# Optimization experiments

Hardware: AMD Instinct MI355X
Metric: run time of the kernel (lower is better)

The kernel has to match this reference:

```python
import jax, jax.numpy as jnp
import numpy as np

N = 50000
E = 800000
F_IN = 128
HID = 128
NCLS = 64


def setup_inputs() -> dict:
    key = jax.random.key(0)
    ks = jax.random.split(key, 10)
    x = jax.random.normal(ks[0], (N, F_IN), dtype=jnp.float32)
    edge_index = jax.random.randint(ks[1], (2, E), 0, N, dtype=jnp.int64)
    def w(k, fi, fo):
        return jax.random.normal(k, (fi, fo), dtype=jnp.float32) / np.sqrt(fi)
    return {
        "x": x,
        "edge_index": edge_index,
        "W1": w(ks[2], F_IN, HID), "b1": jnp.zeros((HID,), jnp.float32),
        "W2": w(ks[3], HID, HID), "b2": jnp.zeros((HID,), jnp.float32),
        "W3": w(ks[4], HID, HID), "b3": jnp.zeros((HID,), jnp.float32),
        "W4": w(ks[5], HID, NCLS), "b4": jnp.zeros((NCLS,), jnp.float32),
    }


def _build_graph(edge_index, n):
    # PyG GCNConv default: add self loops, symmetric normalization D^-1/2 (A+I) D^-1/2
    loops = jnp.arange(n, dtype=edge_index.dtype)
    row = jnp.concatenate([edge_index[0], loops])  # source
    col = jnp.concatenate([edge_index[1], loops])  # destination
    deg = jax.ops.segment_sum(jnp.ones_like(col, dtype=jnp.float32), col, num_segments=n)
    dinv = jnp.where(deg > 0, jax.lax.rsqrt(deg), 0.0)
    norm = dinv[row] * dinv[col]  # [E+N]
    return row, col, norm


def _gcn_layer(x, row, col, norm, W, b, n):
    h = x @ W                                    # [N, out]
    msg = h[row] * norm[:, None]                 # gather + scale, [E+N, out]
    out = jax.ops.segment_sum(msg, col, num_segments=n)  # scatter-add
    return out + b


def reference(x, edge_index, W1, b1, W2, b2, W3, b3, W4, b4):
    n = x.shape[0]
    row, col, norm = _build_graph(edge_index, n)
    h = jax.nn.relu(_gcn_layer(x, row, col, norm, W1, b1, n))
    h = jax.nn.relu(_gcn_layer(h, row, col, norm, W2, b2, n))
    h = jax.nn.relu(_gcn_layer(h, row, col, norm, W3, b3, n))
    return _gcn_layer(h, row, col, norm, W4, b4, n)
```

## Files before the change

### kernel.cpp

```cpp
#include <hip/hip_runtime.h>
#include <hip/hip_fp16.h>
#include <type_traits>

#define N_NODES 50000
#define N_EDGES 800000
#define WIN_BITS 9
#define WIN 512
#define NBUK ((N_NODES + WIN - 1) / WIN)
#define BCAP 16384

typedef _Float16 half8 __attribute__((ext_vector_type(8)));
typedef float floatx4 __attribute__((ext_vector_type(4)));

__global__ __launch_bounds__(256) void p0_bucket(const int* __restrict__ ei,
                                                 int* __restrict__ gcur,
                                                 unsigned* __restrict__ arena, int E) {
    __shared__ int lcnt[NBUK];
    __shared__ int lbase[NBUK];
    int tid = threadIdx.x;
    int chunk = (E + gridDim.x - 1) / gridDim.x;
    int e0 = blockIdx.x * chunk;
    int e1 = e0 + chunk; if (e1 > E) e1 = E;
    for (int b = tid; b < NBUK; b += 256) lcnt[b] = 0;
    __syncthreads();
    for (int e = e0 + tid; e < e1; e += 256) {
        int dst = ei[E + e];
        atomicAdd(&lcnt[dst >> WIN_BITS], 1);
    }
    __syncthreads();
    for (int b = tid; b < NBUK; b += 256) {
        lbase[b] = atomicAdd(&gcur[b], lcnt[b]);
        lcnt[b] = 0;
    }
    __syncthreads();
    for (int e = e0 + tid; e < e1; e += 256) {
        int dst = ei[E + e];
        int src = ei[e];
        int b = dst >> WIN_BITS;
        int pos = lbase[b] + atomicAdd(&lcnt[b], 1);
        if (pos < BCAP)
            arena[(size_t)b * BCAP + pos] = ((unsigned)src << WIN_BITS) | (unsigned)(dst & (WIN - 1));
    }
}

__global__ __launch_bounds__(256) void p1_count(const unsigned* __restrict__ arena,
                                                const int* __restrict__ gcur,
                                                int* __restrict__ deg,
                                                float* __restrict__ dinv, int n) {
    __shared__ int cnt[WIN];
    int b = blockIdx.x, tid = threadIdx.x;
    for (int j = tid; j < WIN; j += 256) cnt[j] = 0;
    __syncthreads();
    int m = gcur[b]; if (m > BCAP) m = BCAP;
    const unsigned* a = arena + (size_t)b * BCAP;
    for (int i = tid; i < m; i += 256) atomicAdd(&cnt[a[i] & (WIN - 1)], 1);
    __syncthreads();
    int base = b << WIN_BITS;
    for (int j = tid; j < WIN; j += 256) {
        int d = base + j;
        if (d < n) {
            int c = cnt[j];
            deg[d] = c;
            dinv[d] = rsqrtf((float)(c + 1));
        }
    }
}

__global__ __launch_bounds__(256) void scan_blocksum(const int* __restrict__ deg,
                                                     int* __restrict__ blocksum, int n) {
    int tid = threadIdx.x;
    int i0 = blockIdx.x * 1024 + tid * 4;
    int4 d = make_int4(0, 0, 0, 0);
    if (i0 + 3 < n) d = *(const int4*)&deg[i0];
    else {
        if (i0 < n)     d.x = deg[i0];
        if (i0 + 1 < n) d.y = deg[i0 + 1];
        if (i0 + 2 < n) d.z = deg[i0 + 2];
        if (i0 + 3 < n) d.w = deg[i0 + 3];
    }
    int s = d.x + d.y + d.z + d.w;
    #pragma unroll
    for (int off = 1; off < 64; off <<= 1) s += __shfl_xor(s, off);
    __shared__ int ws[4];
    if ((tid & 63) == 0) ws[tid >> 6] = s;
    __syncthreads();
    if (tid == 0) blocksum[blockIdx.x] = ws[0] + ws[1] + ws[2] + ws[3];
}

__global__ void scan_blockoff(const int* __restrict__ blocksum, int* __restrict__ blockoff,
                              int nb, int* __restrict__ offsets, int n, int total) {
    int lane = threadIdx.x;
    int v = (lane < nb) ? blocksum[lane] : 0;
    int orig = v;
    #pragma unroll
    for (int off = 1; off < 64; off <<= 1) {
        int t = __shfl_up(v, off);
        if (lane >= off) v += t;
    }
    if (lane < nb) blockoff[lane] = v - orig;
    if (lane == 0) offsets[n] = total;
}

__global__ __launch_bounds__(256) void scan_fill(const int* __restrict__ deg,
                                                 const int* __restrict__ blockoff,
                                                 int* __restrict__ offsets, int n) {
    int tid = threadIdx.x;
    int i0 = blockIdx.x * 1024 + tid * 4;
    int4 d = make_int4(0, 0, 0, 0);
    if (i0 + 3 < n) d = *(const int4*)&deg[i0];
    else {
        if (i0 < n)     d.x = deg[i0];
        if (i0 + 1 < n) d.y = deg[i0 + 1];
        if (i0 + 2 < n) d.z = deg[i0 + 2];
        if (i0 + 3 < n) d.w = deg[i0 + 3];
    }
    int ts = d.x + d.y + d.z + d.w;
    __shared__ int sbuf[256];
    sbuf[tid] = ts;
    __syncthreads();
    #pragma unroll
    for (int off = 1; off < 256; off <<= 1) {
        int t = (tid >= off) ? sbuf[tid - off] : 0;
        __syncthreads();
        sbuf[tid] += t;
        __syncthreads();
    }
    int base = blockoff[blockIdx.x] + (sbuf[tid] - ts);
    int o0 = base, o1 = o0 + d.x, o2 = o1 + d.y, o3 = o2 + d.z;
    if (i0 + 3 < n) {
        *(int4*)&offsets[i0] = make_int4(o0, o1, o2, o3);
    } else {
        if (i0 < n)     offsets[i0]     = o0;
        if (i0 + 1 < n) offsets[i0 + 1] = o1;
        if (i0 + 2 < n) offsets[i0 + 2] = o2;
    }
}

__global__ __launch_bounds__(256) void p2_fill(const unsigned* __restrict__ arena,
                                               const int* __restrict__ gcur,
                                               const int* __restrict__ offsets,
                                               int* __restrict__ csr_src, int n) {
    __shared__ int cur[WIN];
    int b = blockIdx.x, tid = threadIdx.x;
    int base = b << WIN_BITS;
    for (int j = tid; j < WIN; j += 256) {
        int d = base + j;
        cur[j] = (d < n) ? offsets[d] : 0;
    }
    __syncthreads();
    int m = gcur[b]; if (m > BCAP) m = BCAP;
    const unsigned* a = arena + (size_t)b * BCAP;
    for (int i = tid; i < m; i += 256) {
        unsigned e = a[i];
        int pos = atomicAdd(&cur[e & (WIN - 1)], 1);
        csr_src[pos] = (int)(e >> WIN_BITS);
    }
}

template<int FO, typename InT>
__global__ __launch_bounds__(256) void gemm_mfma_kernel(
        const InT* __restrict__ x, const float* __restrict__ W,
        const float* __restrict__ dinv, __half* __restrict__ h, int n) {
    constexpr int NT = FO / 16;
    __shared__ _Float16 wlds[4 * 4 * FO * 8];

    int tid = threadIdx.x;
    constexpr int G = 4 * 4 * FO;
    for (int it = 0; it < G / 256; ++it) {
        int g = tid + it * 256;
        int col = g % FO;
        int sq = g / FO;
        int k0 = sq * 8;
        half8 hv;
        #pragma unroll
        for (int j = 0; j < 8; ++j)
            hv[j] = (_Float16)W[(size_t)(k0 + j) * FO + col];
        *(half8*)&wlds[(size_t)g * 8] = hv;
    }
    __syncthreads();

    int ln = tid & 15;
    int q  = (tid >> 4) & 3;
    int w  = tid >> 6;
    int node = blockIdx.x * 64 + w * 16 + ln;
    int nodec = node < n ? node : n - 1;
    const InT* xrow = x + (size_t)nodec * 128;

    floatx4 acc[NT];
    #pragma unroll
    for (int t = 0; t < NT; ++t) acc[t] = (floatx4){0.f, 0.f, 0.f, 0.f};

    #pragma unroll
    for (int s = 0; s < 4; ++s) {
        half8 xf;
        if constexpr (std::is_same_v<InT, float>) {
            const float* xp = xrow + s * 32 + q * 8;
            float4 a0 = *(const float4*)xp;
            float4 a1 = *(const float4*)(xp + 4);
            xf[0] = (_Float16)a0.x; xf[1] = (_Float16)a0.y;
            xf[2] = (_Float16)a0.z; xf[3] = (_Float16)a0.w;
            xf[4] = (_Float16)a1.x; xf[5] = (_Float16)a1.y;
            xf[6] = (_Float16)a1.z; xf[7] = (_Float16)a1.w;
        } else {
            xf = *(const half8*)(xrow + s * 32 + q * 8);
        }
        int sq = s * 4 + q;
        #pragma unroll
        for (int t = 0; t < NT; ++t) {
            half8 wf = *(const half8*)&wlds[(size_t)(sq * FO + t * 16 + ln) * 8];
            acc[t] = __builtin_amdgcn_mfma_f32_16x16x32_f16(wf, xf, acc[t], 0, 0, 0);
        }
    }

    if (node < n) {
        float dv = dinv[node];
        __half* hrow = h + (size_t)node * FO;
        #pragma unroll
        for (int t = 0; t < NT; ++t) {
            __half2 p[2];
            p[0] = __float22half2_rn(make_float2(acc[t][0] * dv, acc[t][1] * dv));
            p[1] = __float22half2_rn(make_float2(acc[t][2] * dv, acc[t][3] * dv));
            *(uint2*)&hrow[t * 16 + q * 4] = *(const uint2*)p;
        }
    }
}

template<typename OutT, bool RELU>
__global__ __launch_bounds__(256) void agg128_kernel(
        const __half2* __restrict__ h2, const int* __restrict__ offsets,
        const int* __restrict__ csr_src, const float* __restrict__ dinv,
        const float* __restrict__ bias, OutT* __restrict__ out, int n) {
    int lane = threadIdx.x & 63;
    int c = (blockIdx.x << 2) + (threadIdx.x >> 6);
    if (c >= n) return;
    c = __builtin_amdgcn_readfirstlane(c);
    float2 acc = __half22float2(h2[(size_t)c * 64 + lane]);
    int s = offsets[c], e = offsets[c + 1];
    int i = s;
    for (; i + 3 < e; i += 4) {
        int s0 = csr_src[i], s1 = csr_src[i + 1], s2 = csr_src[i + 2], s3 = csr_src[i + 3];
        float2 f0 = __half22float2(h2[(size_t)s0 * 64 + lane]);
        float2 f1 = __half22float2(h2[(size_t)s1 * 64 + lane]);
        float2 f2 = __half22float2(h2[(size_t)s2 * 64 + lane]);
        float2 f3 = __half22float2(h2[(size_t)s3 * 64 + lane]);
        acc.x += f0.x + f1.x; acc.y += f0.y + f1.y;
        acc.x += f2.x + f3.x; acc.y += f2.y + f3.y;
    }
    for (; i < e; ++i) {
        float2 f = __half22float2(h2[(size_t)csr_src[i] * 64 + lane]);
        acc.x += f.x; acc.y += f.y;
    }
    float dc = dinv[c];
    float2 bb = ((const float2*)bias)[lane];
    float vx = fmaf(acc.x, dc, bb.x);
    float vy = fmaf(acc.y, dc, bb.y);
    if (RELU) { vx = fmaxf(vx, 0.0f); vy = fmaxf(vy, 0.0f); }
    if constexpr (std::is_same_v<OutT, __half>) {
        ((__half2*)out)[(size_t)c * 64 + lane] = __float22half2_rn(make_float2(vx, vy));
    } else {
        float2 o; o.x = vx; o.y = vy;
        ((float2*)out)[(size_t)c * 64 + lane] = o;
    }
}

__global__ __launch_bounds__(256) void agg64_kernel(
        const __half2* __restrict__ h2, const int* __restrict__ offsets,
        const int* __restrict__ csr_src, const float* __restrict__ dinv,
        const float* __restrict__ bias, float* __restrict__ out, int n) {
    int lane = threadIdx.x & 63;
    int hf = lane >> 5, sl = lane & 31;
    int c = (blockIdx.x << 2) + (threadIdx.x >> 6);
    if (c >= n) return;
    c = __builtin_amdgcn_readfirstlane(c);
    float2 acc = make_float2(0.0f, 0.0f);
    if (hf == 0) acc = __half22float2(h2[(size_t)c * 32 + sl]);
    int s = offsets[c], e = offsets[c + 1];
    int i = s;
    for (; i + 3 < e; i += 4) {
        int sa = csr_src[i + hf];
        int sb = csr_src[i + 2 + hf];
        float2 fa = __half22float2(h2[(size_t)sa * 32 + sl]);
        float2 fb = __half22float2(h2[(size_t)sb * 32 + sl]);
        acc.x += fa.x + fb.x; acc.y += fa.y + fb.y;
    }
    for (; i + 1 < e; i += 2) {
        int sa = csr_src[i + hf];
        float2 fa = __half22float2(h2[(size_t)sa * 32 + sl]);
        acc.x += fa.x; acc.y += fa.y;
    }
    if (i < e && hf == 0) {
        float2 fa = __half22float2(h2[(size_t)csr_src[i] * 32 + sl]);
        acc.x += fa.x; acc.y += fa.y;
    }
    acc.x += __shfl_xor(acc.x, 32);
    acc.y += __shfl_xor(acc.y, 32);
    if (hf == 0) {
        float dc = dinv[c];
        float2 bb = ((const float2*)bias)[sl];
        float2 o;
        o.x = fmaf(acc.x, dc, bb.x);
        o.y = fmaf(acc.y, dc, bb.y);
        ((float2*)out)[(size_t)c * 32 + sl] = o;
    }
}


extern "C" void kernel_launch(void* const* d_in, const int* in_sizes, int n_in,
                              void* d_out, int out_size, void* d_ws, size_t ws_size,
                              hipStream_t stream) {
    const float* x  = (const float*)d_in[0];
    const int*   ei = (const int*)  d_in[1];
    const float* W1 = (const float*)d_in[2];
    const float* b1 = (const float*)d_in[3];
    const float* W2 = (const float*)d_in[4];
    const float* b2 = (const float*)d_in[5];
    const float* W3 = (const float*)d_in[6];
    const float* b3 = (const float*)d_in[7];
    const float* W4 = (const float*)d_in[8];
    const float* b4 = (const float*)d_in[9];

    const int N = N_NODES, E = N_EDGES;
    const int NSB = (N + 1023) / 1024;

    char* p = (char*)d_ws;
    auto carve = [&](size_t bytes) {
        char* q = p;
        p += (bytes + 255) & ~(size_t)255;
        return (void*)q;
    };
    int*      deg      = (int*)     carve((size_t)N * 4);
    int*      offsets  = (int*)     carve((size_t)(N + 1) * 4);
    int*      csr_src  = (int*)     carve((size_t)E * 4);
    float*    dinv     = (float*)   carve((size_t)N * 4);
    int*      blocksum = (int*)     carve((size_t)NSB * 4);
    int*      blockoff = (int*)     carve((size_t)NSB * 4);
    int*      gcur     = (int*)     carve((size_t)NBUK * 4);
    unsigned* arena    = (unsigned*)carve((size_t)NBUK * BCAP * 4);
    __half*   A        = (__half*)  carve((size_t)N * 128 * 2);
    __half*   B        = (__half*)  carve((size_t)N * 128 * 2);

    hipMemsetAsync(gcur, 0, (size_t)NBUK * 4, stream);
    p0_bucket<<<512, 256, 0, stream>>>(ei, gcur, arena, E);
    p1_count<<<NBUK, 256, 0, stream>>>(arena, gcur, deg, dinv, N);
    scan_blocksum<<<NSB, 256, 0, stream>>>(deg, blocksum, N);
    scan_blockoff<<<1, 64, 0, stream>>>(blocksum, blockoff, NSB, offsets, N, E);
    scan_fill<<<NSB, 256, 0, stream>>>(deg, blockoff, offsets, N);
    p2_fill<<<NBUK, 256, 0, stream>>>(arena, gcur, offsets, csr_src, N);

    const int gemm_grid = (N + 63) / 64;
    const int agg_grid  = (N + 3) / 4;

    gemm_mfma_kernel<128, float><<<gemm_grid, 256, 0, stream>>>(x, W1, dinv, A, N);
    agg128_kernel<__half, true><<<agg_grid, 256, 0, stream>>>((const __half2*)A, offsets, csr_src, dinv, b1, B, N);
    gemm_mfma_kernel<128, __half><<<gemm_grid, 256, 0, stream>>>(B, W2, dinv, A, N);
    agg128_kernel<__half, true><<<agg_grid, 256, 0, stream>>>((const __half2*)A, offsets, csr_src, dinv, b2, B, N);
    gemm_mfma_kernel<128, __half><<<gemm_grid, 256, 0, stream>>>(B, W3, dinv, A, N);
    agg128_kernel<__half, true><<<agg_grid, 256, 0, stream>>>((const __half2*)A, offsets, csr_src, dinv, b3, B, N);
    gemm_mfma_kernel<64, __half><<<gemm_grid, 256, 0, stream>>>(B, W4, dinv, A, N);
    agg64_kernel<<<agg_grid, 256, 0, stream>>>((const __half2*)A, offsets, csr_src, dinv, b4, (float*)d_out, N);
}
```

Before: 312.8 us.

## Fuse aggregation with next-layer MFMA GEMM and merge degree scan into bucket count

Each hidden-layer aggregation (gather-sum, scale, bias, ReLU) now writes its 64-node tile to LDS, and the same 512-thread block runs the next layer's MFMA GEMM on it. This removes the fp16 round trip of the intermediate activations through global memory and three kernel launches. CSR offset construction now scans per-bucket counts in one small kernel and does the per-node prefix inside the count kernel, replacing the three-kernel deg/blocksum/fill scan. The cost is fewer, larger blocks for the gather phase (8 nodes per wave serially), which reduces the memory-level parallelism available to the latency-bound gathers, plus higher LDS use per block.

```diff
diff --git a/kernel.cpp b/kernel.cpp
--- a/kernel.cpp
+++ b/kernel.cpp
@@ -43,96 +43,58 @@
     }
 }
 
-__global__ __launch_bounds__(256) void p1_count(const unsigned* __restrict__ arena,
-                                                const int* __restrict__ gcur,
-                                                int* __restrict__ deg,
-                                                float* __restrict__ dinv, int n) {
+__global__ void scan_buckets(const int* __restrict__ gcur, int* __restrict__ bukoff,
+                             int* __restrict__ offsets, int n, int total) {
+    __shared__ int s[128];
+    int t = threadIdx.x;
+    int v = (t < NBUK) ? gcur[t] : 0;
+    s[t] = v;
+    __syncthreads();
+    for (int off = 1; off < 128; off <<= 1) {
+        int u = (t >= off) ? s[t - off] : 0;
+        __syncthreads();
+        s[t] += u;
+        __syncthreads();
+    }
+    if (t < NBUK) bukoff[t] = s[t] - v;
+    if (t == 0) offsets[n] = total;
+}
+
+__global__ __launch_bounds__(256) void p1_count_scan(const unsigned* __restrict__ arena,
+                                                     const int* __restrict__ gcur,
+                                                     const int* __restrict__ bukoff,
+                                                     int* __restrict__ offsets,
+                                                     float* __restrict__ dinv, int n) {
     __shared__ int cnt[WIN];
+    __shared__ int sbuf[256];
     int b = blockIdx.x, tid = threadIdx.x;
-    for (int j = tid; j < WIN; j += 256) cnt[j] = 0;
+    cnt[tid] = 0; cnt[tid + 256] = 0;
     __syncthreads();
     int m = gcur[b]; if (m > BCAP) m = BCAP;
     const unsigned* a = arena + (size_t)b * BCAP;
     for (int i = tid; i < m; i += 256) atomicAdd(&cnt[a[i] & (WIN - 1)], 1);
     __syncthreads();
+    int j0 = tid * 2;
+    int a0 = cnt[j0], a1 = cnt[j0 + 1];
+    int ts = a0 + a1;
+    sbuf[tid] = ts;
+    __syncthreads();
+    for (int off = 1; off < 256; off <<= 1) {
+        int u = (tid >= off) ? sbuf[tid - off] : 0;
+        __syncthreads();
+        sbuf[tid] += u;
+        __syncthreads();
+    }
+    int pre = sbuf[tid] - ts;
     int base = b << WIN_BITS;
-    for (int j = tid; j < WIN; j += 256) {
-        int d = base + j;
-        if (d < n) {
-            int c = cnt[j];
-            deg[d] = c;
-            dinv[d] = rsqrtf((float)(c + 1));
-        }
-    }
-}
-
-__global__ __launch_bounds__(256) void scan_blocksum(const int* __restrict__ deg,
-                                                     int* __restrict__ blocksum, int n) {
-    int tid = threadIdx.x;
-    int i0 = blockIdx.x * 1024 + tid * 4;
-    int4 d = make_int4(0, 0, 0, 0);
-    if (i0 + 3 < n) d = *(const int4*)&deg[i0];
-    else {
-        if (i0 < n)     d.x = deg[i0];
-        if (i0 + 1 < n) d.y = deg[i0 + 1];
-        if (i0 + 2 < n) d.z = deg[i0 + 2];
-        if (i0 + 3 < n) d.w = deg[i0 + 3];
-    }
-    int s = d.x + d.y + d.z + d.w;
-    #pragma unroll
-    for (int off = 1; off < 64; off <<= 1) s += __shfl_xor(s, off);
-    __shared__ int ws[4];
-    if ((tid & 63) == 0) ws[tid >> 6] = s;
-    __syncthreads();
-    if (tid == 0) blocksum[blockIdx.x] = ws[0] + ws[1] + ws[2] + ws[3];
-}
-
-__global__ void scan_blockoff(const int* __restrict__ blocksum, int* __restrict__ blockoff,
-                              int nb, int* __restrict__ offsets, int n, int total) {
-    int lane = threadIdx.x;
-    int v = (lane < nb) ? blocksum[lane] : 0;
-    int orig = v;
-    #pragma unroll
-    for (int off = 1; off < 64; off <<= 1) {
-        int t = __shfl_up(v, off);
-        if (lane >= off) v += t;
-    }
-    if (lane < nb) blockoff[lane] = v - orig;
-    if (lane == 0) offsets[n] = total;
-}
-
-__global__ __launch_bounds__(256) void scan_fill(const int* __restrict__ deg,
-                                                 const int* __restrict__ blockoff,
-                                                 int* __restrict__ offsets, int n) {
-    int tid = threadIdx.x;
-    int i0 = blockIdx.x * 1024 + tid * 4;
-    int4 d = make_int4(0, 0, 0, 0);
-    if (i0 + 3 < n) d = *(const int4*)&deg[i0];
-    else {
-        if (i0 < n)     d.x = deg[i0];
-        if (i0 + 1 < n) d.y = deg[i0 + 1];
-        if (i0 + 2 < n) d.z = deg[i0 + 2];
-        if (i0 + 3 < n) d.w = deg[i0 + 3];
-    }
-    int ts = d.x + d.y + d.z + d.w;
-    __shared__ int sbuf[256];
-    sbuf[tid] = ts;
-    __syncthreads();
-    #pragma unroll
-    for (int off = 1; off < 256; off <<= 1) {
-        int t = (tid >= off) ? sbuf[tid - off] : 0;
-        __syncthreads();
-        sbuf[tid] += t;
-        __syncthreads();
-    }
-    int base = blockoff[blockIdx.x] + (sbuf[tid] - ts);
-    int o0 = base, o1 = o0 + d.x, o2 = o1 + d.y, o3 = o2 + d.z;
-    if (i0 + 3 < n) {
-        *(int4*)&offsets[i0] = make_int4(o0, o1, o2, o3);
-    } else {
-        if (i0 < n)     offsets[i0]     = o0;
-        if (i0 + 1 < n) offsets[i0 + 1] = o1;
-        if (i0 + 2 < n) offsets[i0 + 2] = o2;
+    int o0 = bukoff[b] + pre, o1 = o0 + a0;
+    int d0 = base + j0;
+    if (d0 + 1 < n) {
+        *(int2*)&offsets[d0] = make_int2(o0, o1);
+        *(float2*)&dinv[d0] = make_float2(rsqrtf((float)(a0 + 1)), rsqrtf((float)(a1 + 1)));
+    } else if (d0 < n) {
+        offsets[d0] = o0;
+        dinv[d0] = rsqrtf((float)(a0 + 1));
     }
 }
 
@@ -162,10 +124,10 @@
         const InT* __restrict__ x, const float* __restrict__ W,
         const float* __restrict__ dinv, __half* __restrict__ h, int n) {
     constexpr int NT = FO / 16;
-    __shared__ _Float16 wlds[4 * 4 * FO * 8];
+    __shared__ _Float16 wlds[16 * FO * 8];
 
     int tid = threadIdx.x;
-    constexpr int G = 4 * 4 * FO;
+    constexpr int G = 16 * FO;
     for (int it = 0; it < G / 256; ++it) {
         int g = tid + it * 256;
         int col = g % FO;
@@ -225,41 +187,95 @@
     }
 }
 
-template<typename OutT, bool RELU>
-__global__ __launch_bounds__(256) void agg128_kernel(
-        const __half2* __restrict__ h2, const int* __restrict__ offsets,
+template<int FO>
+__global__ __launch_bounds__(512) void fused_agg_gemm(
+        const __half2* __restrict__ hin, const int* __restrict__ offsets,
         const int* __restrict__ csr_src, const float* __restrict__ dinv,
-        const float* __restrict__ bias, OutT* __restrict__ out, int n) {
-    int lane = threadIdx.x & 63;
-    int c = (blockIdx.x << 2) + (threadIdx.x >> 6);
-    if (c >= n) return;
-    c = __builtin_amdgcn_readfirstlane(c);
-    float2 acc = __half22float2(h2[(size_t)c * 64 + lane]);
-    int s = offsets[c], e = offsets[c + 1];
-    int i = s;
-    for (; i + 3 < e; i += 4) {
-        int s0 = csr_src[i], s1 = csr_src[i + 1], s2 = csr_src[i + 2], s3 = csr_src[i + 3];
-        float2 f0 = __half22float2(h2[(size_t)s0 * 64 + lane]);
-        float2 f1 = __half22float2(h2[(size_t)s1 * 64 + lane]);
-        float2 f2 = __half22float2(h2[(size_t)s2 * 64 + lane]);
-        float2 f3 = __half22float2(h2[(size_t)s3 * 64 + lane]);
-        acc.x += f0.x + f1.x; acc.y += f0.y + f1.y;
-        acc.x += f2.x + f3.x; acc.y += f2.y + f3.y;
-    }
-    for (; i < e; ++i) {
-        float2 f = __half22float2(h2[(size_t)csr_src[i] * 64 + lane]);
-        acc.x += f.x; acc.y += f.y;
-    }
-    float dc = dinv[c];
+        const float* __restrict__ bias, const float* __restrict__ W,
+        __half* __restrict__ hout, int n) {
+    constexpr int NT  = FO / 16;
+    constexpr int TPW = NT / 2;
+    __shared__ _Float16 wlds[16 * FO * 8];
+    __shared__ _Float16 aggL[64 * 136];
+
+    int tid = threadIdx.x;
+    constexpr int G = 16 * FO;
+    for (int it = 0; it < G / 512; ++it) {
+        int g = tid + it * 512;
+        int col = g % FO;
+        int sq = g / FO;
+        int k0 = sq * 8;
+        half8 hv;
+        #pragma unroll
+        for (int j = 0; j < 8; ++j)
+            hv[j] = (_Float16)W[(size_t)(k0 + j) * FO + col];
+        *(half8*)&wlds[(size_t)g * 8] = hv;
+    }
+
+    int w = tid >> 6;
+    int lane = tid & 63;
     float2 bb = ((const float2*)bias)[lane];
-    float vx = fmaf(acc.x, dc, bb.x);
-    float vy = fmaf(acc.y, dc, bb.y);
-    if (RELU) { vx = fmaxf(vx, 0.0f); vy = fmaxf(vy, 0.0f); }
-    if constexpr (std::is_same_v<OutT, __half>) {
-        ((__half2*)out)[(size_t)c * 64 + lane] = __float22half2_rn(make_float2(vx, vy));
-    } else {
-        float2 o; o.x = vx; o.y = vy;
-        ((float2*)out)[(size_t)c * 64 + lane] = o;
+    __half2* aggRow = (__half2*)aggL;
+    for (int ii = 0; ii < 8; ++ii) {
+        int c = blockIdx.x * 64 + w * 8 + ii;
+        if (c >= n) break;
+        c = __builtin_amdgcn_readfirstlane(c);
+        float2 acc = __half22float2(hin[(size_t)c * 64 + lane]);
+        int s = offsets[c], e = offsets[c + 1];
+        int i = s;
+        for (; i + 3 < e; i += 4) {
+            int s0 = csr_src[i], s1 = csr_src[i + 1], s2 = csr_src[i + 2], s3 = csr_src[i + 3];
+            float2 f0 = __half22float2(hin[(size_t)s0 * 64 + lane]);
+            float2 f1 = __half22float2(hin[(size_t)s1 * 64 + lane]);
+            float2 f2 = __half22float2(hin[(size_t)s2 * 64 + lane]);
+            float2 f3 = __half22float2(hin[(size_t)s3 * 64 + lane]);
+            acc.x += f0.x + f1.x; acc.y += f0.y + f1.y;
+            acc.x += f2.x + f3.x; acc.y += f2.y + f3.y;
+        }
+        for (; i < e; ++i) {
+            float2 f = __half22float2(hin[(size_t)csr_src[i] * 64 + lane]);
+            acc.x += f.x; acc.y += f.y;
+        }
+        float dc = dinv[c];
+        float vx = fmaxf(fmaf(acc.x, dc, bb.x), 0.0f);
+        float vy = fmaxf(fmaf(acc.y, dc, bb.y), 0.0f);
+        aggRow[(size_t)(w * 8 + ii) * 68 + lane] = __float22half2_rn(make_float2(vx, vy));
+    }
+    __syncthreads();
+
+    int ng = w & 3, cg = w >> 2;
+    int ln = tid & 15;
+    int q  = (tid >> 4) & 3;
+    int nl = ng * 16 + ln;
+    int node = blockIdx.x * 64 + nl;
+
+    floatx4 acc[TPW];
+    #pragma unroll
+    for (int t = 0; t < TPW; ++t) acc[t] = (floatx4){0.f, 0.f, 0.f, 0.f};
+
+    #pragma unroll
+    for (int s = 0; s < 4; ++s) {
+        half8 xf = *(const half8*)&aggL[(size_t)nl * 136 + s * 32 + q * 8];
+        int sq = s * 4 + q;
+        #pragma unroll
+        for (int t = 0; t < TPW; ++t) {
+            int T = cg * TPW + t;
+            half8 wf = *(const half8*)&wlds[(size_t)(sq * FO + T * 16 + ln) * 8];
+            acc[t] = __builtin_amdgcn_mfma_f32_16x16x32_f16(wf, xf, acc[t], 0, 0, 0);
+        }
+    }
+
+    if (node < n) {
+        float dv = dinv[node];
+        __half* hrow = hout + (size_t)node * FO;
+        #pragma unroll
+        for (int t = 0; t < TPW; ++t) {
+            int T = cg * TPW + t;
+            __half2 p[2];
+            p[0] = __float22half2_rn(make_float2(acc[t][0] * dv, acc[t][1] * dv));
+            p[1] = __float22half2_rn(make_float2(acc[t][2] * dv, acc[t][3] * dv));
+            *(uint2*)&hrow[T * 16 + q * 4] = *(const uint2*)p;
+        }
     }
 }
 
@@ -320,7 +336,6 @@
     const float* b4 = (const float*)d_in[9];
 
     const int N = N_NODES, E = N_EDGES;
-    const int NSB = (N + 1023) / 1024;
 
     char* p = (char*)d_ws;
     auto carve = [&](size_t bytes) {
@@ -328,34 +343,26 @@
         p += (bytes + 255) & ~(size_t)255;
         return (void*)q;
     };
-    int*      deg      = (int*)     carve((size_t)N * 4);
     int*      offsets  = (int*)     carve((size_t)(N + 1) * 4);
     int*      csr_src  = (int*)     carve((size_t)E * 4);
     float*    dinv     = (float*)   carve((size_t)N * 4);
-    int*      blocksum = (int*)     carve((size_t)NSB * 4);
-    int*      blockoff = (int*)     carve((size_t)NSB * 4);
     int*      gcur     = (int*)     carve((size_t)NBUK * 4);
+    int*      bukoff   = (int*)     carve((size_t)NBUK * 4);
     unsigned* arena    = (unsigned*)carve((size_t)NBUK * BCAP * 4);
-    __half*   A        = (__half*)  carve((size_t)N * 128 * 2);
-    __half*   B        = (__half*)  carve((size_t)N * 128 * 2);
+    __half*   A1       = (__half*)  carve((size_t)N * 128 * 2);
+    __half*   A2       = (__half*)  carve((size_t)N * 128 * 2);
 
     hipMemsetAsync(gcur, 0, (size_t)NBUK * 4, stream);
     p0_bucket<<<512, 256, 0, stream>>>(ei, gcur, arena, E);
-    p1_count<<<NBUK, 256, 0, stream>>>(arena, gcur, deg, dinv, N);
-    scan_blocksum<<<NSB, 256, 0, stream>>>(deg, blocksum, N);
-    scan_blockoff<<<1, 64, 0, stream>>>(blocksum, blockoff, NSB, offsets, N, E);
-    scan_fill<<<NSB, 256, 0, stream>>>(deg, blockoff, offsets, N);
+    scan_buckets<<<1, 128, 0, stream>>>(gcur, bukoff, offsets, N, E);
+    p1_count_scan<<<NBUK, 256, 0, stream>>>(arena, gcur, bukoff, offsets, dinv, N);
     p2_fill<<<NBUK, 256, 0, stream>>>(arena, gcur, offsets, csr_src, N);
 
-    const int gemm_grid = (N + 63) / 64;
-    const int agg_grid  = (N + 3) / 4;
-
-    gemm_mfma_kernel<128, float><<<gemm_grid, 256, 0, stream>>>(x, W1, dinv, A, N);
-    agg128_kernel<__half, true><<<agg_grid, 256, 0, stream>>>((const __half2*)A, offsets, csr_src, dinv, b1, B, N);
-    gemm_mfma_kernel<128, __half><<<gemm_grid, 256, 0, stream>>>(B, W2, dinv, A, N);
-    agg128_kernel<__half, true><<<agg_grid, 256, 0, stream>>>((const __half2*)A, offsets, csr_src, dinv, b2, B, N);
-    gemm_mfma_kernel<128, __half><<<gemm_grid, 256, 0, stream>>>(B, W3, dinv, A, N);
-    agg128_kernel<__half, true><<<agg_grid, 256, 0, stream>>>((const __half2*)A, offsets, csr_src, dinv, b3, B, N);
-    gemm_mfma_kernel<64, __half><<<gemm_grid, 256, 0, stream>>>(B, W4, dinv, A, N);
-    agg64_kernel<<<agg_grid, 256, 0, stream>>>((const __half2*)A, offsets, csr_src, dinv, b4, (float*)d_out, N);
-}
+    const int nb64 = (N + 63) / 64;
+
+    gemm_mfma_kernel<128, float><<<nb64, 256, 0, stream>>>(x, W1, dinv, A1, N);
+    fused_agg_gemm<128><<<nb64, 512, 0, stream>>>((const __half2*)A1, offsets, csr_src, dinv, b1, W2, A2, N);
+    fused_agg_gemm<128><<<nb64, 512, 0, stream>>>((const __half2*)A2, offsets, csr_src, dinv, b2, W3, A1, N);
+    fused_agg_gemm<64><<<nb64, 512, 0, stream>>>((const __half2*)A1, offsets, csr_src, dinv, b3, W4, A2, N);
+    agg64_kernel<<<(N + 3) / 4, 256, 0, stream>>>((const __half2*)A2, offsets, csr_src, dinv, b4, (float*)d_out, N);
+}
```

Result: no change. 314.4 us (+0.5%).
